# Kernel tuning notes

Hardware: AMD Instinct MI355X
Metric: run time of the kernel (lower is better)

## Reference

```python
import jax, jax.numpy as jnp
import numpy as np

N_QUBITS = 12
BATCH = 2048
N_CLASSES = 10


def build_tape(n):
    # 2 layers of: RX on all wires (id 0), RY (id 1), RZ (id 2), then a CRX ring
    # (id 4 forward in layer 0, id 5 reversed in layer 1). 96 gates total for n=12.
    tape = []
    for layer in range(2):
        for i in range(n):
            tape.append(("rx", (i,)))
        for i in range(n):
            tape.append(("ry", (i,)))
        for i in range(n):
            tape.append(("rz", (i,)))
        order = range(n) if layer == 0 else range(n - 1, -1, -1)
        for i in order:
            tape.append(("crx", (i, (i + 1) % n)))
    return tape


def rx_mat(t):
    c = jnp.cos(t / 2).astype(jnp.complex64)
    s = jnp.sin(t / 2).astype(jnp.complex64)
    return jnp.stack([jnp.stack([c, -1j * s]), jnp.stack([-1j * s, c])])


def ry_mat(t):
    c = jnp.cos(t / 2).astype(jnp.complex64)
    s = jnp.sin(t / 2).astype(jnp.complex64)
    return jnp.stack([jnp.stack([c, -s]), jnp.stack([s, c])])


def rz_mat(t):
    em = jnp.exp(-1j * t.astype(jnp.complex64) / 2)
    ep = jnp.exp(1j * t.astype(jnp.complex64) / 2)
    z = jnp.zeros((), jnp.complex64)
    return jnp.stack([jnp.stack([em, z]), jnp.stack([z, ep])])


def apply_1q(psi, U, w):
    # psi: [B] + [2]*n, gate on wire w (axis 1+w)
    psi = jnp.moveaxis(psi, 1 + w, -1)
    psi = psi @ U.T
    return jnp.moveaxis(psi, -1, 1 + w)


def apply_crx(psi, theta, c, t):
    a_c, a_t = 1 + c, 1 + t
    psi = jnp.moveaxis(psi, a_c, 1)  # control -> axis 1
    if a_t < a_c:
        a_t += 1
    psi = jnp.moveaxis(psi, a_t, -1)  # target -> last axis
    U = rx_mat(theta)
    p1 = psi[:, 1] @ U.T  # apply RX only on control=1 branch
    psi = jnp.stack([psi[:, 0], p1], axis=1)
    psi = jnp.moveaxis(psi, -1, a_t)
    return jnp.moveaxis(psi, 1, a_c)


def expvals(psi, n):
    # <X_i>, <Y_i>, <Z_i> for each qubit; returns [B, 3n] ordered X..Y..Z (PL order)
    xs, ys, zs = [], [], []
    for i in range(n):
        p = jnp.moveaxis(psi, 1 + i, -1).reshape(psi.shape[0], -1, 2)
        z = jnp.sum(jnp.abs(p[..., 0]) ** 2 - jnp.abs(p[..., 1]) ** 2, axis=1)
        cross = jnp.sum(jnp.conj(p[..., 0]) * p[..., 1], axis=1)
        xs.append(2.0 * jnp.real(cross))
        ys.append(2.0 * jnp.imag(cross))
        zs.append(jnp.real(z))
    return jnp.stack(xs + ys + zs, axis=1).astype(jnp.float32)


def setup_inputs() -> dict:
    key = jax.random.key(0)
    k0, k1, k2 = jax.random.split(key, 3)
    sv = jax.random.normal(k0, (BATCH, 2 ** N_QUBITS), dtype=jnp.float32)
    sv = sv / jnp.linalg.norm(sv, axis=1, keepdims=True)  # valid quantum states
    n_gates = len(build_tape(N_QUBITS))
    angles = jax.random.normal(k1, (n_gates,), dtype=jnp.float32)
    W = jax.random.normal(k2, (N_CLASSES, 3 * N_QUBITS), dtype=jnp.float32) * 0.1
    b = jnp.zeros((N_CLASSES,), jnp.float32)
    return {"state_vectors": sv, "angles": angles, "W": W, "b": b}


def reference(state_vectors, angles, W, b):
    tape = build_tape(N_QUBITS)
    psi = state_vectors.astype(jnp.complex64).reshape((-1,) + (2,) * N_QUBITS)
    for g, (kind, wires) in enumerate(tape):
        th = angles[g]
        if kind == "rx":
            psi = apply_1q(psi, rx_mat(th), wires[0])
        elif kind == "ry":
            psi = apply_1q(psi, ry_mat(th), wires[0])
        elif kind == "rz":
            psi = apply_1q(psi, rz_mat(th), wires[0])
        else:
            psi = apply_crx(psi, th, wires[0], wires[1])
    feats = expvals(psi, N_QUBITS)  # [B, 3*n_qubits]
    return feats @ W.T + b
```

## Files before the change

### kernel.cpp

```cpp
#include <hip/hip_runtime.h>

#define DIM 4096
using F2 = float2;


__device__ __forceinline__ int addrA(int r, int t) { return (r << 7) | t; }
__device__ __forceinline__ int addrB(int r, int t) { return ((t >> 3) << 8) | (r << 3) | (t & 7); }
__device__ __forceinline__ int addrC(int r, int t) { return ((r & 1) << 11) | (t << 4) | (r >> 1); }
__device__ __forceinline__ int swzAB(int a) { return a ^ ((a >> 5) & 8); }
__device__ __forceinline__ int swzBC(int a) { return a ^ ((a >> 4) & 15) ^ ((a >> 5) & 8); }

__device__ __forceinline__ F2 pk_mul_bl(F2 a, F2 u) {
    F2 d;
    asm("v_pk_mul_f32 %0, %1, %2 op_sel:[0,0] op_sel_hi:[1,0]"
        : "=v"(d) : "v"(a), "v"(u));
    return d;
}
__device__ __forceinline__ void pk_cross(F2& d, F2 a, F2 u) {
    asm("v_pk_fma_f32 %0, %1, %2, %0 op_sel:[1,1,0] op_sel_hi:[0,1,1] neg_lo:[1,0,0]"
        : "+v"(d) : "v"(a), "v"(u));
}
__device__ __forceinline__ void pk_fma_bl(F2& d, F2 a, F2 u) {
    asm("v_pk_fma_f32 %0, %1, %2, %0 op_sel:[0,0,0] op_sel_hi:[1,0,1]"
        : "+v"(d) : "v"(a), "v"(u));
}
__device__ __forceinline__ void pk_swapneg(F2& d, F2 a, F2 cs) {
    asm("v_pk_fma_f32 %0, %1, %2, %0 op_sel:[1,1,0] op_sel_hi:[0,1,1] neg_hi:[1,0,0]"
        : "+v"(d) : "v"(a), "v"(cs));
}
__device__ __forceinline__ void pk_fma(F2& d, F2 a, F2 b) {
    asm("v_pk_fma_f32 %0, %1, %2, %0" : "+v"(d) : "v"(a), "v"(b));
}
__device__ __forceinline__ void pk_imacc(F2& d, F2 a0, F2 a1) {
    asm("v_pk_fma_f32 %0, %1, %2, %0 op_sel:[0,1,0] op_sel_hi:[1,0,1] neg_hi:[1,0,0]"
        : "+v"(d) : "v"(a0), "v"(a1));
}
__device__ __forceinline__ F2 pk_cmul(F2 u, F2 a) {
    F2 d = pk_mul_bl(a, u);
    pk_cross(d, a, u);
    return d;
}
__device__ __forceinline__ void pk_cfma(F2& d, F2 u, F2 a) {
    pk_fma_bl(d, a, u);
    pk_cross(d, a, u);
}

__device__ __forceinline__ void build_u(float tx, float ty, float tz, float* u) {
    float sx = sinf(0.5f*tx), cx = cosf(0.5f*tx);
    float sy = sinf(0.5f*ty), cy = cosf(0.5f*ty);
    float sz = sinf(0.5f*tz), cz = cosf(0.5f*tz);
    float A00r = cy*cx, A00i =  sy*sx;
    float A01r = -sy*cx, A01i = -cy*sx;
    float A10r =  sy*cx, A10i = -cy*sx;
    float A11r =  cy*cx, A11i = -sy*sx;
    u[0] = cz*A00r + sz*A00i;  u[1] = cz*A00i - sz*A00r;
    u[2] = cz*A01r + sz*A01i;  u[3] = cz*A01i - sz*A01r;
    u[4] = cz*A10r - sz*A10i;  u[5] = cz*A10i + sz*A10r;
    u[6] = cz*A11r - sz*A11i;  u[7] = cz*A11i + sz*A11r;
}

__global__ void prep_kernel(const float* __restrict__ ang, float* __restrict__ coef) {
    int t = threadIdx.x;
    if (t < 12) {
        float u[8]; build_u(ang[t], ang[12+t], ang[24+t], u);
#pragma unroll
        for (int j = 0; j < 8; ++j) coef[t*8 + j] = u[j];
    } else if (t < 24) {
        int q = t - 12;
        float u[8]; build_u(ang[48+q], ang[60+q], ang[72+q], u);
#pragma unroll
        for (int j = 0; j < 8; ++j) coef[192 + q*8 + j] = u[j];
    } else if (t < 36) {
        int c = t - 24;
        float th = 0.5f * ang[95 - c];
        coef[296 + c*2]     = cosf(th);
        coef[296 + c*2 + 1] = sinf(th);
    } else if (t < 47) {
        int q = t - 35;
        float u[8]; build_u(ang[q], ang[12+q], ang[24+q], u);
        float c = cosf(0.5f*ang[36+q-1]), s = sinf(0.5f*ang[36+q-1]);
        float m[8];
        m[0] = c*u[0] + s*u[5];  m[1] = c*u[1] - s*u[4];
        m[2] = c*u[2] + s*u[7];  m[3] = c*u[3] - s*u[6];
        m[4] = s*u[1] + c*u[4];  m[5] = -s*u[0] + c*u[5];
        m[6] = s*u[3] + c*u[6];  m[7] = -s*u[2] + c*u[7];
#pragma unroll
        for (int j = 0; j < 8; ++j) coef[96 + q*8 + j] = m[j];
    } else if (t == 47) {
        float u[8]; build_u(ang[48], ang[60], ang[72], u);
        float c = cosf(0.5f*ang[47]), s = sinf(0.5f*ang[47]);
        float m[8];
        m[0] = c*u[0] + s*u[3];  m[1] = c*u[1] - s*u[2];
        m[2] = s*u[1] + c*u[2];  m[3] = -s*u[0] + c*u[3];
        m[4] = c*u[4] + s*u[7];  m[5] = c*u[5] - s*u[6];
        m[6] = s*u[5] + c*u[6];  m[7] = -s*u[4] + c*u[7];
#pragma unroll
        for (int j = 0; j < 8; ++j) coef[288 + j] = m[j];
    }
}

template<int M>
__device__ __forceinline__ void g1q(F2* amp, const float* __restrict__ u) {
    F2 u00 = {u[0], u[1]}, u01 = {u[2], u[3]};
    F2 u10 = {u[4], u[5]}, u11 = {u[6], u[7]};
#pragma unroll
    for (int r0 = 0; r0 < 32; ++r0) {
        if (r0 & M) continue;
        const int r1 = r0 + M;
        F2 a0 = amp[r0], a1 = amp[r1];
        F2 n0 = pk_cmul(u00, a0); pk_cfma(n0, u01, a1);
        F2 n1 = pk_cmul(u10, a0); pk_cfma(n1, u11, a1);
        amp[r0] = n0; amp[r1] = n1;
    }
}

template<int MSEL, int M>
__device__ __forceinline__ void fg1q(F2* amp, const float* __restrict__ uA,
                                     const float* __restrict__ uB) {
    F2 a00 = {uA[0], uA[1]}, a01 = {uA[2], uA[3]}, a10 = {uA[4], uA[5]}, a11 = {uA[6], uA[7]};
    F2 b00 = {uB[0], uB[1]}, b01 = {uB[2], uB[3]}, b10 = {uB[4], uB[5]}, b11 = {uB[6], uB[7]};
#pragma unroll
    for (int r0 = 0; r0 < 32; ++r0) {
        if (r0 & M) continue;
        const int r1 = r0 + M;
        const bool sel = (r0 & MSEL) != 0;
        F2 u00 = sel ? b00 : a00, u01 = sel ? b01 : a01;
        F2 u10 = sel ? b10 : a10, u11 = sel ? b11 : a11;
        F2 a0 = amp[r0], a1 = amp[r1];
        F2 n0 = pk_cmul(u00, a0); pk_cfma(n0, u01, a1);
        F2 n1 = pk_cmul(u10, a0); pk_cfma(n1, u11, a1);
        amp[r0] = n0; amp[r1] = n1;
    }
}

template<int MC, int MT>
__device__ __forceinline__ void crx(F2* amp, F2 cs) {
#pragma unroll
    for (int r0 = 0; r0 < 32; ++r0) {
        if (!(r0 & MC) || (r0 & MT)) continue;
        const int r1 = r0 + MT;
        F2 a0 = amp[r0], a1 = amp[r1];
        F2 n0 = pk_mul_bl(a0, cs); pk_swapneg(n0, a1, cs);
        F2 n1 = pk_mul_bl(a1, cs); pk_swapneg(n1, a0, cs);
        amp[r0] = n0; amp[r1] = n1;
    }
}

template<int M>
__device__ __forceinline__ void expv(const F2* amp, int q, int lane,
                                     float& fx, float& fy, float& fz) {
    F2 zp = {0.f, 0.f}, zm = {0.f, 0.f}, xp = {0.f, 0.f}, ip = {0.f, 0.f};
#pragma unroll
    for (int r0 = 0; r0 < 32; ++r0) {
        if (r0 & M) continue;
        const int r1 = r0 + M;
        F2 a0 = amp[r0], a1 = amp[r1];
        pk_fma(zp, a0, a0);
        pk_fma(zm, a1, a1);
        pk_fma(xp, a0, a1);
        pk_imacc(ip, a0, a1);
    }
    float zz = (zp.x + zp.y) - (zm.x + zm.y);
    float xr = 2.f * (xp.x + xp.y);
    float xi = 2.f * (ip.x + ip.y);
#pragma unroll
    for (int off = 32; off; off >>= 1) {
        xr += __shfl_xor(xr, off);
        xi += __shfl_xor(xi, off);
        zz += __shfl_xor(zz, off);
    }
    if (lane == q) { fx = xr; fy = xi; fz = zz; }
}

#define XPOSE(CUR, NXT, SWZ) \
  { _Pragma("unroll") for (int r = 0; r < 32; ++r) psi[SWZ(CUR(r, t))] = amp[r]; \
    __syncthreads(); \
    _Pragma("unroll") for (int r = 0; r < 32; ++r) amp[r] = psi[SWZ(NXT(r, t))]; \
    __syncthreads(); }

#define U0P(q, M)        g1q<M>(amp, cf + (q)*8)
#define FU0(q, MSEL, M)  fg1q<MSEL, M>(amp, cf + (q)*8, cf + 96 + (q)*8)
#define U1P(q, M)        g1q<M>(amp, cf + 192 + (q)*8)
#define FU1_0()          fg1q<2, 1>(amp, cf + 192, cf + 288)
#define CR1(c, MC, MT)   crx<MC, MT>(amp, F2{cf[296 + (c)*2], cf[296 + (c)*2 + 1]})
#define EXPV(q, M)       expv<M>(amp, q, lane, fx, fy, fz)

__global__ __launch_bounds__(128, 1)
void qsim_kernel(const float* __restrict__ sv,
                 const float* __restrict__ cf,
                 const float* __restrict__ W,
                 const float* __restrict__ bvec,
                 float* __restrict__ out)
{
    __shared__ F2 psi[DIM];
    const int t = threadIdx.x;
    const int b = blockIdx.x;
    const int lane = t & 63, w = t >> 6;

    F2 amp[32];
    const float* svb = sv + (size_t)b * DIM;
#pragma unroll
    for (int r = 0; r < 32; ++r)
        amp[r] = make_float2(svb[(r << 7) | t], 0.f);

    float fx = 0.f, fy = 0.f, fz = 0.f;

    U0P(0, 16);
    FU0(1, 16, 8); FU0(2, 8, 4); FU0(3, 4, 2); FU0(4, 2, 1);
    XPOSE(addrA, addrB, swzAB);

    FU0(5, 16, 8); FU0(6, 8, 4); FU0(7, 4, 2); FU0(8, 2, 1);
    XPOSE(addrB, addrC, swzBC);

    FU0(9, 16, 8); FU0(10, 8, 4); FU0(11, 4, 2);
    FU1_0();
    U1P(8, 16); U1P(9, 8); U1P(10, 4); U1P(11, 2);
    CR1(11, 2, 1); CR1(10, 4, 2); CR1(9, 8, 4); CR1(8, 16, 8);
    EXPV(9, 8); EXPV(10, 4); EXPV(11, 2);
    XPOSE(addrC, addrB, swzBC);

    U1P(4, 16); U1P(5, 8); U1P(6, 4); U1P(7, 2);
    CR1(7, 2, 1); CR1(6, 4, 2); CR1(5, 8, 4); CR1(4, 16, 8);
    EXPV(5, 8); EXPV(6, 4); EXPV(7, 2); EXPV(8, 1);
    XPOSE(addrB, addrA, swzAB);

    U1P(1, 8); U1P(2, 4); U1P(3, 2);
    CR1(3, 2, 1); CR1(2, 4, 2); CR1(1, 8, 4); CR1(0, 16, 8);
    EXPV(0, 16); EXPV(1, 8); EXPV(2, 4); EXPV(3, 2); EXPV(4, 1);

    float* fbuf = (float*)psi;
    if (lane < 12) {
        fbuf[w * 36 + lane]      = fx;
        fbuf[w * 36 + 12 + lane] = fy;
        fbuf[w * 36 + 24 + lane] = fz;
    }
    __syncthreads();
    if (t < 10) {
        float a = bvec[t];
#pragma unroll
        for (int f = 0; f < 36; ++f)
            a += W[t * 36 + f] * (fbuf[f] + fbuf[36 + f]);
        out[(size_t)b * 10 + t] = a;
    }
}

extern "C" void kernel_launch(void* const* d_in, const int* in_sizes, int n_in,
                              void* d_out, int out_size, void* d_ws, size_t ws_size,
                              hipStream_t stream) {
    const float* sv     = (const float*)d_in[0];
    const float* angles = (const float*)d_in[1];
    const float* W      = (const float*)d_in[2];
    const float* bvec   = (const float*)d_in[3];
    float* out  = (float*)d_out;
    float* coef = (float*)d_ws;
    int batch = in_sizes[0] / DIM;
    prep_kernel<<<1, 64, 0, stream>>>(angles, coef);
    qsim_kernel<<<batch, 128, 0, stream>>>(sv, coef, W, bvec, out);
}
```

Baseline: 135.7 us.

## Halve shared memory by transposing state vector in two half passes

Shared scratch for the qubit-axis transposes shrinks from the full 4096-amplitude state to half of it. Each transpose now runs as two passes, each moving the 16 register slots that share one chosen bit, and the register-to-qubit mapping and gate stride arguments are permuted to match. The smaller LDS footprint is meant to let more workgroups fit per CU, raising occupancy and latency hiding. The cost is twice as many barriers per transpose and more complex index math.

```diff
diff --git a/kernel.cpp b/kernel.cpp
--- a/kernel.cpp
+++ b/kernel.cpp
@@ -4,11 +4,18 @@
 using F2 = float2;
 
 
-__device__ __forceinline__ int addrA(int r, int t) { return (r << 7) | t; }
-__device__ __forceinline__ int addrB(int r, int t) { return ((t >> 3) << 8) | (r << 3) | (t & 7); }
-__device__ __forceinline__ int addrC(int r, int t) { return ((r & 1) << 11) | (t << 4) | (r >> 1); }
-__device__ __forceinline__ int swzAB(int a) { return a ^ ((a >> 5) & 8); }
-__device__ __forceinline__ int swzBC(int a) { return a ^ ((a >> 4) & 15) ^ ((a >> 5) & 8); }
+__device__ __forceinline__ int swzb(int i) { return i ^ ((i >> 6) & 15); }
+__device__ __forceinline__ int ampA(int s, int t) { return (s << 7) | t; }
+__device__ __forceinline__ int ampB(int s, int t) {
+    int r = ((s >> 1) & 15) | ((s & 1) << 4);
+    return ((t >> 3) << 8) | (r << 3) | (t & 7);
+}
+__device__ __forceinline__ int ampC(int u, int t) {
+    return ((u & 1) << 11) | (t << 4) | (((u >> 1) & 1) << 3) |
+           (((u >> 4) & 1) << 2) | (((u >> 3) & 1) << 1) | ((u >> 2) & 1);
+}
+__device__ __forceinline__ int bx7(int a) { return ((a >> 8) << 7) | (a & 127); }
+__device__ __forceinline__ int bx3(int a) { return ((a >> 4) << 3) | (a & 7); }
 
 __device__ __forceinline__ F2 pk_mul_bl(F2 a, F2 u) {
     F2 d;
@@ -172,16 +179,22 @@
     if (lane == q) { fx = xr; fy = xi; fz = zz; }
 }
 
-#define XPOSE(CUR, NXT, SWZ) \
-  { _Pragma("unroll") for (int r = 0; r < 32; ++r) psi[SWZ(CUR(r, t))] = amp[r]; \
-    __syncthreads(); \
-    _Pragma("unroll") for (int r = 0; r < 32; ++r) amp[r] = psi[SWZ(NXT(r, t))]; \
-    __syncthreads(); }
+#define XP2(SB, SRC, BXS, DST, BXD) \
+  { _Pragma("unroll") \
+    for (int h = 0; h < 2; ++h) { \
+      _Pragma("unroll") \
+      for (int s = 0; s < 32; ++s) \
+        if (((s >> SB) & 1) == h) buf[swzb(BXS(SRC(s, t)))] = amp[s]; \
+      __syncthreads(); \
+      _Pragma("unroll") \
+      for (int s = 0; s < 32; ++s) \
+        if (((s >> SB) & 1) == h) amp[s] = buf[swzb(BXD(DST(s, t)))]; \
+      __syncthreads(); \
+    } }
 
 #define U0P(q, M)        g1q<M>(amp, cf + (q)*8)
 #define FU0(q, MSEL, M)  fg1q<MSEL, M>(amp, cf + (q)*8, cf + 96 + (q)*8)
 #define U1P(q, M)        g1q<M>(amp, cf + 192 + (q)*8)
-#define FU1_0()          fg1q<2, 1>(amp, cf + 192, cf + 288)
 #define CR1(c, MC, MT)   crx<MC, MT>(amp, F2{cf[296 + (c)*2], cf[296 + (c)*2 + 1]})
 #define EXPV(q, M)       expv<M>(amp, q, lane, fx, fy, fz)
 
@@ -192,7 +205,7 @@
                  const float* __restrict__ bvec,
                  float* __restrict__ out)
 {
-    __shared__ F2 psi[DIM];
+    __shared__ F2 buf[DIM / 2];
     const int t = threadIdx.x;
     const int b = blockIdx.x;
     const int lane = t & 63, w = t >> 6;
@@ -207,28 +220,28 @@
 
     U0P(0, 16);
     FU0(1, 16, 8); FU0(2, 8, 4); FU0(3, 4, 2); FU0(4, 2, 1);
-    XPOSE(addrA, addrB, swzAB);
-
-    FU0(5, 16, 8); FU0(6, 8, 4); FU0(7, 4, 2); FU0(8, 2, 1);
-    XPOSE(addrB, addrC, swzBC);
-
-    FU0(9, 16, 8); FU0(10, 8, 4); FU0(11, 4, 2);
-    FU1_0();
-    U1P(8, 16); U1P(9, 8); U1P(10, 4); U1P(11, 2);
-    CR1(11, 2, 1); CR1(10, 4, 2); CR1(9, 8, 4); CR1(8, 16, 8);
-    EXPV(9, 8); EXPV(10, 4); EXPV(11, 2);
-    XPOSE(addrC, addrB, swzBC);
-
-    U1P(4, 16); U1P(5, 8); U1P(6, 4); U1P(7, 2);
-    CR1(7, 2, 1); CR1(6, 4, 2); CR1(5, 8, 4); CR1(4, 16, 8);
-    EXPV(5, 8); EXPV(6, 4); EXPV(7, 2); EXPV(8, 1);
-    XPOSE(addrB, addrA, swzAB);
+    XP2(0, ampA, bx7, ampB, bx7);
+
+    FU0(5, 1, 16); FU0(6, 16, 8); FU0(7, 8, 4); FU0(8, 4, 2);
+    XP2(1, ampB, bx3, ampC, bx3);
+
+    FU0(9, 2, 16); FU0(10, 16, 8); FU0(11, 8, 4);
+    fg1q<4, 1>(amp, cf + 192, cf + 288);
+    U1P(8, 2); U1P(9, 16); U1P(10, 8); U1P(11, 4);
+    CR1(11, 4, 1); CR1(10, 8, 4); CR1(9, 16, 8); CR1(8, 2, 16);
+    EXPV(9, 16); EXPV(10, 8); EXPV(11, 4);
+    XP2(1, ampC, bx3, ampB, bx3);
+
+    U1P(4, 1); U1P(5, 16); U1P(6, 8); U1P(7, 4);
+    CR1(7, 4, 2); CR1(6, 8, 4); CR1(5, 16, 8); CR1(4, 1, 16);
+    EXPV(5, 16); EXPV(6, 8); EXPV(7, 4); EXPV(8, 2);
+    XP2(0, ampB, bx7, ampA, bx7);
 
     U1P(1, 8); U1P(2, 4); U1P(3, 2);
     CR1(3, 2, 1); CR1(2, 4, 2); CR1(1, 8, 4); CR1(0, 16, 8);
     EXPV(0, 16); EXPV(1, 8); EXPV(2, 4); EXPV(3, 2); EXPV(4, 1);
 
-    float* fbuf = (float*)psi;
+    float* fbuf = (float*)buf;
     if (lane < 12) {
         fbuf[w * 36 + lane]      = fx;
         fbuf[w * 36 + 12 + lane] = fy;
```

Measured after the change: 161.0 us. +18.6%, slower.

## Process two state vectors per block, interleaving compute with LDS transposes

Applied to the files above, without the earlier changes.

Each block now simulates two batch samples held in two register arrays. The shared-memory transpose of one sample is interleaved with gate compute on the other, so the barrier and LDS latency of one can be hidden behind the ALU work of the other. The grid is halved. The cost is doubled register pressure (64 float2 amplitudes per thread), which risks spills at launch_bounds(128,1). The kernel also now assumes an even batch size.

```diff
diff --git a/kernel.cpp b/kernel.cpp
--- a/kernel.cpp
+++ b/kernel.cpp
@@ -172,18 +172,35 @@
     if (lane == q) { fx = xr; fy = xi; fz = zz; }
 }
 
-#define XPOSE(CUR, NXT, SWZ) \
-  { _Pragma("unroll") for (int r = 0; r < 32; ++r) psi[SWZ(CUR(r, t))] = amp[r]; \
-    __syncthreads(); \
-    _Pragma("unroll") for (int r = 0; r < 32; ++r) amp[r] = psi[SWZ(NXT(r, t))]; \
-    __syncthreads(); }
-
-#define U0P(q, M)        g1q<M>(amp, cf + (q)*8)
-#define FU0(q, MSEL, M)  fg1q<MSEL, M>(amp, cf + (q)*8, cf + 96 + (q)*8)
-#define U1P(q, M)        g1q<M>(amp, cf + 192 + (q)*8)
-#define FU1_0()          fg1q<2, 1>(amp, cf + 192, cf + 288)
-#define CR1(c, MC, MT)   crx<MC, MT>(amp, F2{cf[296 + (c)*2], cf[296 + (c)*2 + 1]})
-#define EXPV(q, M)       expv<M>(amp, q, lane, fx, fy, fz)
+#define ST(A, ADDR, SWZ) \
+  { _Pragma("unroll") for (int r = 0; r < 32; ++r) psi[SWZ(ADDR(r, t))] = A[r]; }
+#define LDR(A, ADDR, SWZ) \
+  { _Pragma("unroll") for (int r = 0; r < 32; ++r) A[r] = psi[SWZ(ADDR(r, t))]; }
+
+#define U0P(A, q, M)        g1q<M>(A, cf + (q)*8)
+#define FU0(A, q, MS, M)    fg1q<MS, M>(A, cf + (q)*8, cf + 96 + (q)*8)
+#define U1P(A, q, M)        g1q<M>(A, cf + 192 + (q)*8)
+#define CR1(A, c, MC, MT)   crx<MC, MT>(A, F2{cf[296 + (c)*2], cf[296 + (c)*2 + 1]})
+#define EXPV(A, q, M, FX, FY, FZ)  expv<M>(A, q, lane, FX, FY, FZ)
+
+#define GA(A)        { U0P(A,0,16); FU0(A,1,16,8); FU0(A,2,8,4); FU0(A,3,4,2); FU0(A,4,2,1); }
+#define GB_1(A)      { FU0(A,5,16,8); FU0(A,6,8,4); }
+#define GB_2(A)      { FU0(A,7,4,2); FU0(A,8,2,1); }
+#define GC_1(A)      { FU0(A,9,16,8); FU0(A,10,8,4); FU0(A,11,4,2); \
+                       fg1q<2,1>(A, cf + 192, cf + 288); U1P(A,8,16); }
+#define GC_2(A,FX,FY,FZ) { U1P(A,9,8); U1P(A,10,4); U1P(A,11,2); \
+                       CR1(A,11,2,1); CR1(A,10,4,2); CR1(A,9,8,4); CR1(A,8,16,8); \
+                       EXPV(A,9,8,FX,FY,FZ); EXPV(A,10,4,FX,FY,FZ); EXPV(A,11,2,FX,FY,FZ); }
+#define GBP_1(A)     { U1P(A,4,16); U1P(A,5,8); }
+#define GBP_2(A,FX,FY,FZ) { U1P(A,6,4); U1P(A,7,2); \
+                       CR1(A,7,2,1); CR1(A,6,4,2); CR1(A,5,8,4); CR1(A,4,16,8); \
+                       EXPV(A,5,8,FX,FY,FZ); EXPV(A,6,4,FX,FY,FZ); \
+                       EXPV(A,7,2,FX,FY,FZ); EXPV(A,8,1,FX,FY,FZ); }
+#define GAP_1(A)     { U1P(A,1,8); U1P(A,2,4); }
+#define GAP_2(A,FX,FY,FZ) { U1P(A,3,2); \
+                       CR1(A,3,2,1); CR1(A,2,4,2); CR1(A,1,8,4); CR1(A,0,16,8); \
+                       EXPV(A,0,16,FX,FY,FZ); EXPV(A,1,8,FX,FY,FZ); EXPV(A,2,4,FX,FY,FZ); \
+                       EXPV(A,3,2,FX,FY,FZ); EXPV(A,4,1,FX,FY,FZ); }
 
 __global__ __launch_bounds__(128, 1)
 void qsim_kernel(const float* __restrict__ sv,
@@ -194,53 +211,95 @@
 {
     __shared__ F2 psi[DIM];
     const int t = threadIdx.x;
-    const int b = blockIdx.x;
+    const int b0 = blockIdx.x * 2;
     const int lane = t & 63, w = t >> 6;
 
-    F2 amp[32];
-    const float* svb = sv + (size_t)b * DIM;
-#pragma unroll
-    for (int r = 0; r < 32; ++r)
-        amp[r] = make_float2(svb[(r << 7) | t], 0.f);
-
-    float fx = 0.f, fy = 0.f, fz = 0.f;
-
-    U0P(0, 16);
-    FU0(1, 16, 8); FU0(2, 8, 4); FU0(3, 4, 2); FU0(4, 2, 1);
-    XPOSE(addrA, addrB, swzAB);
-
-    FU0(5, 16, 8); FU0(6, 8, 4); FU0(7, 4, 2); FU0(8, 2, 1);
-    XPOSE(addrB, addrC, swzBC);
-
-    FU0(9, 16, 8); FU0(10, 8, 4); FU0(11, 4, 2);
-    FU1_0();
-    U1P(8, 16); U1P(9, 8); U1P(10, 4); U1P(11, 2);
-    CR1(11, 2, 1); CR1(10, 4, 2); CR1(9, 8, 4); CR1(8, 16, 8);
-    EXPV(9, 8); EXPV(10, 4); EXPV(11, 2);
-    XPOSE(addrC, addrB, swzBC);
-
-    U1P(4, 16); U1P(5, 8); U1P(6, 4); U1P(7, 2);
-    CR1(7, 2, 1); CR1(6, 4, 2); CR1(5, 8, 4); CR1(4, 16, 8);
-    EXPV(5, 8); EXPV(6, 4); EXPV(7, 2); EXPV(8, 1);
-    XPOSE(addrB, addrA, swzAB);
-
-    U1P(1, 8); U1P(2, 4); U1P(3, 2);
-    CR1(3, 2, 1); CR1(2, 4, 2); CR1(1, 8, 4); CR1(0, 16, 8);
-    EXPV(0, 16); EXPV(1, 8); EXPV(2, 4); EXPV(3, 2); EXPV(4, 1);
+    F2 amp1[32], amp2[32];
+    const float* svb = sv + (size_t)b0 * DIM;
+#pragma unroll
+    for (int r = 0; r < 32; ++r) amp1[r] = make_float2(svb[(r << 7) | t], 0.f);
+#pragma unroll
+    for (int r = 0; r < 32; ++r) amp2[r] = make_float2(svb[DIM + ((r << 7) | t)], 0.f);
+
+    float fx1 = 0.f, fy1 = 0.f, fz1 = 0.f;
+    float fx2 = 0.f, fy2 = 0.f, fz2 = 0.f;
+
+    GA(amp1);
+    ST(amp1, addrA, swzAB);
+    GA(amp2);
+    __syncthreads();
+    LDR(amp1, addrB, swzAB);
+    GB_1(amp1);
+    __syncthreads();
+    ST(amp2, addrA, swzAB);
+    GB_2(amp1);
+    __syncthreads();
+    LDR(amp2, addrB, swzAB);
+    GB_1(amp2);
+    __syncthreads();
+
+    ST(amp1, addrB, swzBC);
+    GB_2(amp2);
+    __syncthreads();
+    LDR(amp1, addrC, swzBC);
+    GC_1(amp1);
+    __syncthreads();
+    ST(amp2, addrB, swzBC);
+    GC_2(amp1, fx1, fy1, fz1);
+    __syncthreads();
+    LDR(amp2, addrC, swzBC);
+    GC_1(amp2);
+    __syncthreads();
+
+    ST(amp1, addrC, swzBC);
+    GC_2(amp2, fx2, fy2, fz2);
+    __syncthreads();
+    LDR(amp1, addrB, swzBC);
+    GBP_1(amp1);
+    __syncthreads();
+    ST(amp2, addrC, swzBC);
+    GBP_2(amp1, fx1, fy1, fz1);
+    __syncthreads();
+    LDR(amp2, addrB, swzBC);
+    GBP_1(amp2);
+    __syncthreads();
+
+    ST(amp1, addrB, swzAB);
+    GBP_2(amp2, fx2, fy2, fz2);
+    __syncthreads();
+    LDR(amp1, addrA, swzAB);
+    GAP_1(amp1);
+    __syncthreads();
+    ST(amp2, addrB, swzAB);
+    GAP_2(amp1, fx1, fy1, fz1);
+    __syncthreads();
+    LDR(amp2, addrA, swzAB);
+    GAP_1(amp2); GAP_2(amp2, fx2, fy2, fz2);
+    __syncthreads();
 
     float* fbuf = (float*)psi;
     if (lane < 12) {
-        fbuf[w * 36 + lane]      = fx;
-        fbuf[w * 36 + 12 + lane] = fy;
-        fbuf[w * 36 + 24 + lane] = fz;
+        fbuf[w*36 + lane]            = fx1;
+        fbuf[w*36 + 12 + lane]       = fy1;
+        fbuf[w*36 + 24 + lane]       = fz1;
+        fbuf[(2+w)*36 + lane]        = fx2;
+        fbuf[(2+w)*36 + 12 + lane]   = fy2;
+        fbuf[(2+w)*36 + 24 + lane]   = fz2;
     }
     __syncthreads();
     if (t < 10) {
         float a = bvec[t];
 #pragma unroll
         for (int f = 0; f < 36; ++f)
-            a += W[t * 36 + f] * (fbuf[f] + fbuf[36 + f]);
-        out[(size_t)b * 10 + t] = a;
+            a += W[t*36 + f] * (fbuf[f] + fbuf[36 + f]);
+        out[(size_t)b0*10 + t] = a;
+    } else if (t >= 64 && t < 74) {
+        int c = t - 64;
+        float a = bvec[c];
+#pragma unroll
+        for (int f = 0; f < 36; ++f)
+            a += W[c*36 + f] * (fbuf[72 + f] + fbuf[108 + f]);
+        out[(size_t)(b0 + 1)*10 + c] = a;
     }
 }
 
@@ -255,5 +314,5 @@
     float* coef = (float*)d_ws;
     int batch = in_sizes[0] / DIM;
     prep_kernel<<<1, 64, 0, stream>>>(angles, coef);
-    qsim_kernel<<<batch, 128, 0, stream>>>(sv, coef, W, bvec, out);
-}
+    qsim_kernel<<<batch / 2, 128, 0, stream>>>(sv, coef, W, bvec, out);
+}
```

Result: slower. 176.2 us (+29.8%).

## Split statevector across 256 threads with 16 amplitudes each and extra transposes

Applied to the files above, without the earlier changes.

Each block now runs 256 threads that each hold 16 amplitudes instead of 128 threads holding 32. This lowers register pressure and raises occupancy and latency hiding. The gate schedule is re-planned around a new four-layout transpose sequence (A/B/C/D) with a simple XOR swizzle. The cost is more LDS transpose rounds and barriers, and a four-wave feature reduction in the final linear layer.

```diff
diff --git a/kernel.cpp b/kernel.cpp
--- a/kernel.cpp
+++ b/kernel.cpp
@@ -4,11 +4,11 @@
 using F2 = float2;
 
 
-__device__ __forceinline__ int addrA(int r, int t) { return (r << 7) | t; }
-__device__ __forceinline__ int addrB(int r, int t) { return ((t >> 3) << 8) | (r << 3) | (t & 7); }
-__device__ __forceinline__ int addrC(int r, int t) { return ((r & 1) << 11) | (t << 4) | (r >> 1); }
-__device__ __forceinline__ int swzAB(int a) { return a ^ ((a >> 5) & 8); }
-__device__ __forceinline__ int swzBC(int a) { return a ^ ((a >> 4) & 15) ^ ((a >> 5) & 8); }
+__device__ __forceinline__ int swz(int i)          { return i ^ (i >> 6); }
+__device__ __forceinline__ int addrA(int r, int t) { return (r << 8) | t; }
+__device__ __forceinline__ int addrB(int r, int t) { return ((t >> 5) << 9) | (r << 5) | (t & 31); }
+__device__ __forceinline__ int addrC(int r, int t) { return ((t >> 2) << 6) | (r << 2) | (t & 3); }
+__device__ __forceinline__ int addrD(int r, int t) { return ((r >> 3) << 11) | (t << 3) | (r & 7); }
 
 __device__ __forceinline__ F2 pk_mul_bl(F2 a, F2 u) {
     F2 d;
@@ -104,7 +104,7 @@
     F2 u00 = {u[0], u[1]}, u01 = {u[2], u[3]};
     F2 u10 = {u[4], u[5]}, u11 = {u[6], u[7]};
 #pragma unroll
-    for (int r0 = 0; r0 < 32; ++r0) {
+    for (int r0 = 0; r0 < 16; ++r0) {
         if (r0 & M) continue;
         const int r1 = r0 + M;
         F2 a0 = amp[r0], a1 = amp[r1];
@@ -120,7 +120,7 @@
     F2 a00 = {uA[0], uA[1]}, a01 = {uA[2], uA[3]}, a10 = {uA[4], uA[5]}, a11 = {uA[6], uA[7]};
     F2 b00 = {uB[0], uB[1]}, b01 = {uB[2], uB[3]}, b10 = {uB[4], uB[5]}, b11 = {uB[6], uB[7]};
 #pragma unroll
-    for (int r0 = 0; r0 < 32; ++r0) {
+    for (int r0 = 0; r0 < 16; ++r0) {
         if (r0 & M) continue;
         const int r1 = r0 + M;
         const bool sel = (r0 & MSEL) != 0;
@@ -136,7 +136,7 @@
 template<int MC, int MT>
 __device__ __forceinline__ void crx(F2* amp, F2 cs) {
 #pragma unroll
-    for (int r0 = 0; r0 < 32; ++r0) {
+    for (int r0 = 0; r0 < 16; ++r0) {
         if (!(r0 & MC) || (r0 & MT)) continue;
         const int r1 = r0 + MT;
         F2 a0 = amp[r0], a1 = amp[r1];
@@ -151,7 +151,7 @@
                                      float& fx, float& fy, float& fz) {
     F2 zp = {0.f, 0.f}, zm = {0.f, 0.f}, xp = {0.f, 0.f}, ip = {0.f, 0.f};
 #pragma unroll
-    for (int r0 = 0; r0 < 32; ++r0) {
+    for (int r0 = 0; r0 < 16; ++r0) {
         if (r0 & M) continue;
         const int r1 = r0 + M;
         F2 a0 = amp[r0], a1 = amp[r1];
@@ -172,20 +172,19 @@
     if (lane == q) { fx = xr; fy = xi; fz = zz; }
 }
 
-#define XPOSE(CUR, NXT, SWZ) \
-  { _Pragma("unroll") for (int r = 0; r < 32; ++r) psi[SWZ(CUR(r, t))] = amp[r]; \
+#define XPOSE(CUR, NXT) \
+  { _Pragma("unroll") for (int r = 0; r < 16; ++r) psi[swz(CUR(r, t))] = amp[r]; \
     __syncthreads(); \
-    _Pragma("unroll") for (int r = 0; r < 32; ++r) amp[r] = psi[SWZ(NXT(r, t))]; \
+    _Pragma("unroll") for (int r = 0; r < 16; ++r) amp[r] = psi[swz(NXT(r, t))]; \
     __syncthreads(); }
 
-#define U0P(q, M)        g1q<M>(amp, cf + (q)*8)
-#define FU0(q, MSEL, M)  fg1q<MSEL, M>(amp, cf + (q)*8, cf + 96 + (q)*8)
-#define U1P(q, M)        g1q<M>(amp, cf + 192 + (q)*8)
-#define FU1_0()          fg1q<2, 1>(amp, cf + 192, cf + 288)
-#define CR1(c, MC, MT)   crx<MC, MT>(amp, F2{cf[296 + (c)*2], cf[296 + (c)*2 + 1]})
-#define EXPV(q, M)       expv<M>(amp, q, lane, fx, fy, fz)
-
-__global__ __launch_bounds__(128, 1)
+#define U0P(q, M)       g1q<M>(amp, cf + (q)*8)
+#define FU0(q, MS, M)   fg1q<MS, M>(amp, cf + (q)*8, cf + 96 + (q)*8)
+#define U1P(q, M)       g1q<M>(amp, cf + 192 + (q)*8)
+#define CR1(c, MC, MT)  crx<MC, MT>(amp, F2{cf[296 + (c)*2], cf[296 + (c)*2 + 1]})
+#define EXPV(q, M)      expv<M>(amp, q, lane, fx, fy, fz)
+
+__global__ __launch_bounds__(256, 1)
 void qsim_kernel(const float* __restrict__ sv,
                  const float* __restrict__ cf,
                  const float* __restrict__ W,
@@ -197,36 +196,45 @@
     const int b = blockIdx.x;
     const int lane = t & 63, w = t >> 6;
 
-    F2 amp[32];
+    F2 amp[16];
     const float* svb = sv + (size_t)b * DIM;
 #pragma unroll
-    for (int r = 0; r < 32; ++r)
-        amp[r] = make_float2(svb[(r << 7) | t], 0.f);
+    for (int r = 0; r < 16; ++r)
+        amp[r] = make_float2(svb[(r << 8) | t], 0.f);
 
     float fx = 0.f, fy = 0.f, fz = 0.f;
 
-    U0P(0, 16);
-    FU0(1, 16, 8); FU0(2, 8, 4); FU0(3, 4, 2); FU0(4, 2, 1);
-    XPOSE(addrA, addrB, swzAB);
-
-    FU0(5, 16, 8); FU0(6, 8, 4); FU0(7, 4, 2); FU0(8, 2, 1);
-    XPOSE(addrB, addrC, swzBC);
-
-    FU0(9, 16, 8); FU0(10, 8, 4); FU0(11, 4, 2);
-    FU1_0();
-    U1P(8, 16); U1P(9, 8); U1P(10, 4); U1P(11, 2);
-    CR1(11, 2, 1); CR1(10, 4, 2); CR1(9, 8, 4); CR1(8, 16, 8);
-    EXPV(9, 8); EXPV(10, 4); EXPV(11, 2);
-    XPOSE(addrC, addrB, swzBC);
-
-    U1P(4, 16); U1P(5, 8); U1P(6, 4); U1P(7, 2);
-    CR1(7, 2, 1); CR1(6, 4, 2); CR1(5, 8, 4); CR1(4, 16, 8);
-    EXPV(5, 8); EXPV(6, 4); EXPV(7, 2); EXPV(8, 1);
-    XPOSE(addrB, addrA, swzAB);
-
-    U1P(1, 8); U1P(2, 4); U1P(3, 2);
-    CR1(3, 2, 1); CR1(2, 4, 2); CR1(1, 8, 4); CR1(0, 16, 8);
-    EXPV(0, 16); EXPV(1, 8); EXPV(2, 4); EXPV(3, 2); EXPV(4, 1);
+    U0P(0, 8);
+    FU0(1, 8, 4); FU0(2, 4, 2); FU0(3, 2, 1);
+    XPOSE(addrA, addrB);
+
+    FU0(4, 8, 4); FU0(5, 4, 2); FU0(6, 2, 1);
+    XPOSE(addrB, addrC);
+
+    FU0(7, 8, 4); FU0(8, 4, 2); FU0(9, 2, 1);
+    XPOSE(addrC, addrD);
+
+    FU0(10, 4, 2); FU0(11, 2, 1);
+    fg1q<1, 8>(amp, cf + 192, cf + 288);
+    U1P(9, 4); U1P(10, 2); U1P(11, 1);
+    CR1(11, 1, 8); CR1(10, 2, 1); CR1(9, 4, 2);
+    EXPV(10, 2); EXPV(11, 1);
+    XPOSE(addrD, addrC);
+
+    U1P(6, 8); U1P(7, 4); U1P(8, 2);
+    CR1(8, 2, 1); CR1(7, 4, 2); CR1(6, 8, 4);
+    EXPV(9, 1); EXPV(8, 2); EXPV(7, 4);
+    XPOSE(addrC, addrB);
+
+    U1P(3, 8); U1P(4, 4); U1P(5, 2);
+    CR1(5, 2, 1); CR1(4, 4, 2); CR1(3, 8, 4);
+    EXPV(6, 1); EXPV(5, 2); EXPV(4, 4);
+    XPOSE(addrB, addrA);
+
+    U1P(1, 4); U1P(2, 2);
+    CR1(2, 2, 1); CR1(1, 4, 2); CR1(0, 8, 4);
+    EXPV(0, 8); EXPV(1, 4); EXPV(2, 2); EXPV(3, 1);
+    __syncthreads();
 
     float* fbuf = (float*)psi;
     if (lane < 12) {
@@ -239,7 +247,7 @@
         float a = bvec[t];
 #pragma unroll
         for (int f = 0; f < 36; ++f)
-            a += W[t * 36 + f] * (fbuf[f] + fbuf[36 + f]);
+            a += W[t * 36 + f] * (fbuf[f] + fbuf[36 + f] + fbuf[72 + f] + fbuf[108 + f]);
         out[(size_t)b * 10 + t] = a;
     }
 }
@@ -255,5 +263,5 @@
     float* coef = (float*)d_ws;
     int batch = in_sizes[0] / DIM;
     prep_kernel<<<1, 64, 0, stream>>>(angles, coef);
-    qsim_kernel<<<batch, 128, 0, stream>>>(sv, coef, W, bvec, out);
-}
+    qsim_kernel<<<batch, 256, 0, stream>>>(sv, coef, W, bvec, out);
+}
```

New measurement: 147.1 us. 8.4% more time.
